# Kernel optimization log

Measured on AMD Instinct MI355X. Metric: run time of the kernel, lower is better.

The kernel has to match this reference:

```python
import jax, jax.numpy as jnp
import numpy as np

BN_EPS = 1e-5

def _bn(x, g, b, m, v):
    # eval-mode BatchNorm1d over channel dim of [B, C, N]
    scale = g / jnp.sqrt(v + BN_EPS)
    return (x - m[:, None]) * scale[:, None] + b[:, None]

def _conv1(W, x, b=None):
    # 1x1 Conv1d == channel matmul: W [O, C], x [B, C, N] -> [B, O, N]
    y = jnp.einsum('oc,bcn->bon', W, x)
    if b is not None:
        y = y + b[:, None]
    return y

def _sa_layer(x, wqk, wv, bv, wt, bt, g, b, m, v):
    # offset self-attention; q_conv and k_conv share weights
    xk = _conv1(wqk, x)                          # [B, D, N]
    xq = jnp.swapaxes(xk, 1, 2)                  # [B, N, D]
    xv = _conv1(wv, x, bv)                       # [B, D, N]
    energy = jnp.einsum('bnd,bdm->bnm', xq, xk)  # [B, N, N]
    attn = jax.nn.softmax(energy, axis=-1)
    attn = attn / (1e-9 + attn.sum(axis=1, keepdims=True))  # L1 renorm over dim=1
    x_r = jnp.einsum('bdn,bnm->bdm', xv, attn)   # [B, D, N]
    x_r = jax.nn.relu(_bn(_conv1(wt, x - x_r, bt), g, b, m, v))
    return x + x_r

def setup_inputs() -> dict:
    key = jax.random.key(0)
    ks = iter(jax.random.split(key, 64))
    B, Cin, N = 16, 3, 2048
    D, F, H1, OUT = 128, 1024, 512, 50
    def rn(shape, s=0.05):
        return jax.random.normal(next(ks), shape, dtype=jnp.float32) * s
    def var(shape):
        return jax.random.uniform(next(ks), shape, dtype=jnp.float32) * 0.5 + 0.5
    inp = {
        'x': jax.random.normal(next(ks), (B, Cin, N), dtype=jnp.float32),
        'w1': rn((D, Cin)), 'w2': rn((D, D)),
        'bn1_g': jnp.ones((D,)), 'bn1_b': jnp.zeros((D,)), 'bn1_m': rn((D,)), 'bn1_v': var((D,)),
        'bn2_g': jnp.ones((D,)), 'bn2_b': jnp.zeros((D,)), 'bn2_m': rn((D,)), 'bn2_v': var((D,)),
        'sa_wqk': rn((4, D, D)), 'sa_wv': rn((4, D, D)), 'sa_bv': rn((4, D)),
        'sa_wt': rn((4, D, D)), 'sa_bt': rn((4, D)),
        'sa_g': jnp.ones((4, D)), 'sa_b': jnp.zeros((4, D)), 'sa_m': rn((4, D)), 'sa_v': var((4, D)),
        'wf': rn((F, 4 * D)),
        'bnf_g': jnp.ones((F,)), 'bnf_b': jnp.zeros((F,)), 'bnf_m': rn((F,)), 'bnf_v': var((F,)),
        'ws1': rn((H1, 3 * F)), 'bs1': rn((H1,)),
        'bns1_g': jnp.ones((H1,)), 'bns1_b': jnp.zeros((H1,)), 'bns1_m': rn((H1,)), 'bns1_v': var((H1,)),
        'ws2': rn((OUT, H1)), 'bs2': rn((OUT,)),
        'bns2_g': jnp.ones((OUT,)), 'bns2_b': jnp.zeros((OUT,)), 'bns2_m': rn((OUT,)), 'bns2_v': var((OUT,)),
    }
    return inp

def reference(x, w1, w2, bn1_g, bn1_b, bn1_m, bn1_v, bn2_g, bn2_b, bn2_m, bn2_v,
              sa_wqk, sa_wv, sa_bv, sa_wt, sa_bt, sa_g, sa_b, sa_m, sa_v,
              wf, bnf_g, bnf_b, bnf_m, bnf_v,
              ws1, bs1, bns1_g, bns1_b, bns1_m, bns1_v,
              ws2, bs2, bns2_g, bns2_b, bns2_m, bns2_v):
    B, _, N = x.shape
    h = jax.nn.relu(_bn(_conv1(w1, x), bn1_g, bn1_b, bn1_m, bn1_v))
    h = jax.nn.relu(_bn(_conv1(w2, h), bn2_g, bn2_b, bn2_m, bn2_v))
    feats = []
    for i in range(4):
        h = _sa_layer(h, sa_wqk[i], sa_wv[i], sa_bv[i], sa_wt[i], sa_bt[i],
                      sa_g[i], sa_b[i], sa_m[i], sa_v[i])
        feats.append(h)
    cat = jnp.concatenate(feats, axis=1)                 # [B, 512, N]
    fused = _bn(_conv1(wf, cat), bnf_g, bnf_b, bnf_m, bnf_v)
    fused = jnp.where(fused >= 0, fused, 0.2 * fused)    # LeakyReLU(0.2)
    x_max = fused.max(axis=2)                            # [B, 1024]
    x_avg = fused.mean(axis=2)                           # [B, 1024]
    gmax = jnp.broadcast_to(x_max[:, :, None], (B, x_max.shape[1], N))
    gavg = jnp.broadcast_to(x_avg[:, :, None], (B, x_avg.shape[1], N))
    h = jnp.concatenate([fused, gmax, gavg], axis=1)     # [B, 3072, N]
    h = jax.nn.relu(_bn(_conv1(ws1, h, bs1), bns1_g, bns1_b, bns1_m, bns1_v))
    # dropout is identity in eval mode
    h = jax.nn.relu(_bn(_conv1(ws2, h, bs2), bns2_g, bns2_b, bns2_m, bns2_v))
    return h  # [B, out_channel, N]
```

## Files before the change

### kernel.cpp

```cpp
#include <hip/hip_runtime.h>
#include <cstdint>
#include <cstddef>

#define B_   16
#define N_   2048
#define D_   128
#define F_   1024
#define H1_  512
#define OUT_ 50

static constexpr float BN_EPS = 1e-5f;

typedef __attribute__((ext_vector_type(8))) short short8;
typedef __attribute__((ext_vector_type(4))) float f32x4;

__device__ inline unsigned short f2bf(float f) {
  union { float f; unsigned u; } v; v.f = f;
  unsigned r = v.u + 0x7fff + ((v.u >> 16) & 1);
  return (unsigned short)(r >> 16);
}

__device__ inline void dma16(const unsigned short* g, unsigned short* l) {
  __builtin_amdgcn_global_load_lds(
      (const __attribute__((address_space(1))) unsigned int*)g,
      (__attribute__((address_space(3))) unsigned int*)l, 16, 0, 0);
}

__global__ void foldw_k(const float* __restrict__ W, int ldW,
                        const float* __restrict__ bias,
                        const float* __restrict__ g, const float* __restrict__ bb,
                        const float* __restrict__ m, const float* __restrict__ v,
                        unsigned short* __restrict__ Wb, float* __restrict__ biasF,
                        int O, int Opad, int K) {
  long i = (long)blockIdx.x * 256 + threadIdx.x;
  if (i >= (long)Opad * K) return;
  int o = (int)(i / K), k = (int)(i % K);
  float sc = 1.f, sh = 0.f;
  if (o < O && g) { sc = g[o] * rsqrtf(v[o] + BN_EPS); sh = bb[o] - m[o] * sc; }
  float w = (o < O) ? W[(long)o * ldW + k] * sc : 0.f;
  Wb[i] = f2bf(w);
  if (k == 0 && biasF) {
    float bf = 0.f;
    if (o < O) bf = (bias ? bias[o] : 0.f) * sc + sh;
    biasF[o] = bf;
  }
}

__global__ void conv1_k(const float* __restrict__ x, const float* __restrict__ w1,
                        const float* __restrict__ g, const float* __restrict__ bb,
                        const float* __restrict__ m, const float* __restrict__ v,
                        unsigned short* __restrict__ h0b) {
  int o = threadIdx.x, n = blockIdx.x, b = blockIdx.y;
  const float* xb = x + (long)b * 3 * N_;
  float val = w1[o * 3 + 0] * xb[n] + w1[o * 3 + 1] * xb[N_ + n] + w1[o * 3 + 2] * xb[2 * N_ + n];
  float sc = g[o] * rsqrtf(v[o] + BN_EPS);
  val = val * sc + (bb[o] - m[o] * sc);
  h0b[((long)b * N_ + n) * D_ + o] = f2bf(fmaxf(val, 0.f));
}

template <int TM>
__global__ __launch_bounds__(256, 4)
void gemm_tok(const unsigned short* __restrict__ Wb, int ldW,
              const unsigned short* __restrict__ A, long sA, int ldA,
              const float* __restrict__ biasF,
              const float* __restrict__ perBO, int ldPBO,
              const float* __restrict__ res, long sRes, int ldRes,
              float* __restrict__ outF, long sOutF, int ldOutF,
              unsigned short* __restrict__ outH, long sOutH, int ldOutH,
              float* __restrict__ pmax, float* __restrict__ psum,
              int K, int act, int flags) {
  constexpr int MT = TM / 32;
  __shared__ unsigned short lA[TM * 64];
  __shared__ unsigned short lB[128 * 64];
  __shared__ float lpm[4][64], lps[4][64];
  int tid = threadIdx.x;
  int n0 = blockIdx.x * TM, o0 = blockIdx.y * 128, b = blockIdx.z;
  int wave = tid >> 6, lane = tid & 63;
  int wr = wave >> 1, wc = wave & 1;
  int quad = lane >> 4, l15 = lane & 15;
  int rowL = lane >> 3;
  int kseg = (lane & 7) ^ rowL;
  const unsigned short* Ab = A + (long)b * sA + (long)n0 * ldA;
  const unsigned short* Wp = Wb + (long)o0 * ldW;

  f32x4 acc[MT][4];
  #pragma unroll
  for (int i = 0; i < MT; ++i)
    #pragma unroll
    for (int j = 0; j < 4; ++j) acc[i][j] = (f32x4){0.f, 0.f, 0.f, 0.f};

  for (int kc = 0; kc < K; kc += 64) {
    #pragma unroll
    for (int t = 0; t < 4; ++t) {
      int chunk = t * 4 + wave;
      dma16(Wp + (long)(chunk * 8 + rowL) * ldW + kc + kseg * 8, &lB[chunk * 512]);
      if (chunk < TM / 8)
        dma16(Ab + (long)(chunk * 8 + rowL) * ldA + kc + kseg * 8, &lA[chunk * 512]);
    }
    __syncthreads();
    #pragma unroll
    for (int kk = 0; kk < 2; ++kk) {
      short8 af[MT], bf[4];
      #pragma unroll
      for (int mt = 0; mt < MT; ++mt) {
        int r = wr * (TM / 2) + mt * 16 + l15;
        af[mt] = *(const short8*)&lA[r * 64 + (((kk * 4 + quad) ^ (l15 & 7)) * 8)];
      }
      #pragma unroll
      for (int ot = 0; ot < 4; ++ot) {
        int r = wc * 64 + ot * 16 + l15;
        bf[ot] = *(const short8*)&lB[r * 64 + (((kk * 4 + quad) ^ (l15 & 7)) * 8)];
      }
      #pragma unroll
      for (int mt = 0; mt < MT; ++mt)
        #pragma unroll
        for (int ot = 0; ot < 4; ++ot)
          acc[mt][ot] = __builtin_amdgcn_mfma_f32_16x16x32_bf16(bf[ot], af[mt], acc[mt][ot], 0, 0, 0);
    }
    __syncthreads();
  }

  bool doPool = (flags & 32) != 0;
  #pragma unroll
  for (int ot = 0; ot < 4; ++ot) {
    int ob = o0 + wc * 64 + ot * 16 + quad * 4;
    float bi[4] = {0.f, 0.f, 0.f, 0.f};
    if (biasF) { float4 t = *(const float4*)&biasF[ob]; bi[0] = t.x; bi[1] = t.y; bi[2] = t.z; bi[3] = t.w; }
    if (perBO) {
      float4 t = *(const float4*)&perBO[(long)b * ldPBO + ob];
      bi[0] += t.x; bi[1] += t.y; bi[2] += t.z; bi[3] += t.w;
    }
    float pm4[4], ps4[4];
    #pragma unroll
    for (int r = 0; r < 4; ++r) { pm4[r] = -1e30f; ps4[r] = 0.f; }
    #pragma unroll
    for (int mt = 0; mt < MT; ++mt) {
      int n = n0 + wr * (TM / 2) + mt * 16 + l15;
      float vals[4];
      #pragma unroll
      for (int r = 0; r < 4; ++r) {
        float val = acc[mt][ot][r] + bi[r];
        if (act == 1)      val = fmaxf(val, 0.f);
        else if (act == 2) val = (val >= 0.f) ? val : 0.2f * val;
        vals[r] = val;
      }
      if (flags & 16) {
        float4 t = *(const float4*)&res[(long)b * sRes + (long)n * ldRes + ob];
        vals[0] += t.x; vals[1] += t.y; vals[2] += t.z; vals[3] += t.w;
      }
      if (flags & 1)
        *(float4*)&outF[(long)b * sOutF + (long)n * ldOutF + ob] = *(float4*)vals;
      {
        unsigned short t[4];
        #pragma unroll
        for (int r = 0; r < 4; ++r) t[r] = f2bf(vals[r]);
        *(uint2*)&outH[(long)b * sOutH + (long)n * ldOutH + ob] = *(uint2*)&t[0];
      }
      if (doPool) {
        #pragma unroll
        for (int r = 0; r < 4; ++r) { pm4[r] = fmaxf(pm4[r], vals[r]); ps4[r] += vals[r]; }
      }
    }
    if (doPool) {
      #pragma unroll
      for (int r = 0; r < 4; ++r) {
        float m = pm4[r], s = ps4[r];
        m = fmaxf(m, __shfl_xor(m, 1)); s += __shfl_xor(s, 1);
        m = fmaxf(m, __shfl_xor(m, 2)); s += __shfl_xor(s, 2);
        m = fmaxf(m, __shfl_xor(m, 4)); s += __shfl_xor(s, 4);
        m = fmaxf(m, __shfl_xor(m, 8)); s += __shfl_xor(s, 8);
        if (l15 == 0) { lpm[wave][ot * 16 + quad * 4 + r] = m; lps[wave][ot * 16 + quad * 4 + r] = s; }
      }
    }
  }
  if (doPool) {
    __syncthreads();
    if (tid < 128) {
      int wcx = tid >> 6, ol = tid & 63;
      float m = fmaxf(lpm[wcx][ol], lpm[wcx + 2][ol]);
      float s = lps[wcx][ol] + lps[wcx + 2][ol];
      int o = o0 + wcx * 64 + ol;
      pmax[((long)b * 16 + blockIdx.x) * 1024 + o] = m;
      psum[((long)b * 16 + blockIdx.x) * 1024 + o] = s;
    }
  }
}

template <int TM>
__global__ __launch_bounds__(256, 4)
void gemm_chan(const unsigned short* __restrict__ Wb, int ldW,
               const unsigned short* __restrict__ A, long sA, int ldA,
               const float* __restrict__ biasF,
               float* __restrict__ outF, long sOutF, int ldOutF,
               unsigned short* __restrict__ outH, long sOutH, int ldOutH,
               int K, int O, int act) {
  constexpr int MT = TM / 32;
  __shared__ unsigned short lA[TM * 64];
  __shared__ unsigned short lB[128 * 64];
  int tid = threadIdx.x;
  int n0 = blockIdx.x * TM, o0 = blockIdx.y * 128, b = blockIdx.z;
  int wave = tid >> 6, lane = tid & 63;
  int wr = wave >> 1, wc = wave & 1;
  int quad = lane >> 4, l15 = lane & 15;
  int rowL = lane >> 3;
  int kseg = (lane & 7) ^ rowL;
  const unsigned short* Ab = A + (long)b * sA + (long)n0 * ldA;
  const unsigned short* Wp = Wb + (long)o0 * ldW;

  f32x4 acc[MT][4];
  #pragma unroll
  for (int i = 0; i < MT; ++i)
    #pragma unroll
    for (int j = 0; j < 4; ++j) acc[i][j] = (f32x4){0.f, 0.f, 0.f, 0.f};

  for (int kc = 0; kc < K; kc += 64) {
    #pragma unroll
    for (int t = 0; t < 4; ++t) {
      int chunk = t * 4 + wave;
      dma16(Wp + (long)(chunk * 8 + rowL) * ldW + kc + kseg * 8, &lB[chunk * 512]);
      if (chunk < TM / 8)
        dma16(Ab + (long)(chunk * 8 + rowL) * ldA + kc + kseg * 8, &lA[chunk * 512]);
    }
    __syncthreads();
    #pragma unroll
    for (int kk = 0; kk < 2; ++kk) {
      short8 af[MT], bf[4];
      #pragma unroll
      for (int mt = 0; mt < MT; ++mt) {
        int r = wr * (TM / 2) + mt * 16 + l15;
        af[mt] = *(const short8*)&lA[r * 64 + (((kk * 4 + quad) ^ (l15 & 7)) * 8)];
      }
      #pragma unroll
      for (int ot = 0; ot < 4; ++ot) {
        int r = wc * 64 + ot * 16 + l15;
        bf[ot] = *(const short8*)&lB[r * 64 + (((kk * 4 + quad) ^ (l15 & 7)) * 8)];
      }
      #pragma unroll
      for (int mt = 0; mt < MT; ++mt)
        #pragma unroll
        for (int ot = 0; ot < 4; ++ot)
          acc[mt][ot] = __builtin_amdgcn_mfma_f32_16x16x32_bf16(af[mt], bf[ot], acc[mt][ot], 0, 0, 0);
    }
    __syncthreads();
  }

  #pragma unroll
  for (int ot = 0; ot < 4; ++ot) {
    int o = o0 + wc * 64 + ot * 16 + l15;
    if (o >= O) continue;
    float bi = biasF ? biasF[o] : 0.f;
    #pragma unroll
    for (int mt = 0; mt < MT; ++mt) {
      int nb = n0 + wr * (TM / 2) + mt * 16 + quad * 4;
      float vals[4];
      #pragma unroll
      for (int r = 0; r < 4; ++r) {
        float val = acc[mt][ot][r] + bi;
        if (act == 1)      val = fmaxf(val, 0.f);
        else if (act == 2) val = (val >= 0.f) ? val : 0.2f * val;
        vals[r] = val;
      }
      if (outF)
        *(float4*)&outF[(long)b * sOutF + (long)o * ldOutF + nb] = *(float4*)vals;
      if (outH) {
        unsigned short t[4];
        #pragma unroll
        for (int r = 0; r < 4; ++r) t[r] = f2bf(vals[r]);
        *(uint2*)&outH[(long)b * sOutH + (long)o * ldOutH + nb] = *(uint2*)&t[0];
      }
    }
  }
}

__global__ __launch_bounds__(256)
void gram_lw(const unsigned short* __restrict__ xk, long sXk,
             float* __restrict__ lw) {
  __shared__ unsigned short lK[64 * 128];
  int tid = threadIdx.x, wave = tid >> 6, lane = tid & 63;
  int quad = lane >> 4, l15 = lane & 15;
  int rowL4 = lane >> 4, s16 = lane & 15;
  int n0 = blockIdx.x * 64, b = blockIdx.y;
  const unsigned short* Kp = xk + (long)b * sXk;
  short8 afr[4];
  {
    const unsigned short* arow = Kp + (long)(n0 + wave * 16 + l15) * 128;
    #pragma unroll
    for (int kf = 0; kf < 4; ++kf) afr[kf] = *(const short8*)(arow + kf * 32 + quad * 8);
  }
  float runm[4], runs[4];
  #pragma unroll
  for (int r = 0; r < 4; ++r) { runm[r] = -1e30f; runs[r] = 0.f; }

  for (int m0 = 0; m0 < 2048; m0 += 64) {
    __syncthreads();
    #pragma unroll
    for (int t = 0; t < 4; ++t) {
      int c = t * 4 + wave;
      int row = c * 4 + rowL4;
      int gseg = (s16 & 8) | ((s16 ^ (row & 7)) & 7);
      dma16(Kp + (long)(m0 + row) * 128 + gseg * 8, &lK[c * 512]);
    }
    __syncthreads();
    #pragma unroll
    for (int mf = 0; mf < 4; ++mf) {
      f32x4 s = (f32x4){0.f, 0.f, 0.f, 0.f};
      #pragma unroll
      for (int kf = 0; kf < 4; ++kf) {
        int r = mf * 16 + l15, q = kf * 4 + quad;
        int sp = (q & 8) | ((q ^ (r & 7)) & 7);
        short8 bfr = *(const short8*)&lK[r * 128 + sp * 8];
        s = __builtin_amdgcn_mfma_f32_16x16x32_bf16(afr[kf], bfr, s, 0, 0, 0);
      }
      #pragma unroll
      for (int r = 0; r < 4; ++r) {
        float e = s[r];
        float mn = fmaxf(runm[r], e);
        runs[r] = runs[r] * __expf(runm[r] - mn) + __expf(e - mn);
        runm[r] = mn;
      }
    }
  }
  #pragma unroll
  for (int r = 0; r < 4; ++r) {
    float m = runm[r], s = runs[r];
    #pragma unroll
    for (int off = 1; off < 16; off <<= 1) {
      float mo = __shfl_xor(m, off), so = __shfl_xor(s, off);
      float mn = fmaxf(m, mo);
      s = s * __expf(m - mn) + so * __expf(mo - mn);
      m = mn;
    }
    if (l15 == 0) {
      int n = n0 + wave * 16 + quad * 4 + r;
      lw[(long)b * 2048 + n] = m + __logf(s);
    }
  }
}

__global__ __launch_bounds__(256)
void pv_k(const unsigned short* __restrict__ xk, long sXk,
          const unsigned short* __restrict__ xv, long sXv,
          const float* __restrict__ lw,
          const float* __restrict__ li, long sLi, int ldLi,
          unsigned short* __restrict__ xrb, long sXr) {
  __shared__ unsigned short lK[64 * 128];
  __shared__ unsigned short lV[128 * 64];
  __shared__ unsigned short lP[4][16 * 72];
  __shared__ float lwt[64];
  int tid = threadIdx.x, wave = tid >> 6, lane = tid & 63;
  int quad = lane >> 4, l15 = lane & 15;
  int rowL4 = lane >> 4, s16 = lane & 15;
  int rowL8 = lane >> 3, s8 = lane & 7;
  int m0 = blockIdx.x * 64, b = blockIdx.y;
  const unsigned short* Kp = xk + (long)b * sXk;
  const unsigned short* Vp = xv + (long)b * sXv;
  short8 akr[4];
  {
    const unsigned short* arow = Kp + (long)(m0 + wave * 16 + l15) * 128;
    #pragma unroll
    for (int kf = 0; kf < 4; ++kf) akr[kf] = *(const short8*)(arow + kf * 32 + quad * 8);
  }
  f32x4 acc[8];
  #pragma unroll
  for (int dt = 0; dt < 8; ++dt) acc[dt] = (f32x4){0.f, 0.f, 0.f, 0.f};
  float runc[4] = {0.f, 0.f, 0.f, 0.f};

  for (int n0c = 0; n0c < 2048; n0c += 64) {
    __syncthreads();
    #pragma unroll
    for (int t = 0; t < 4; ++t) {
      int cK = t * 4 + wave;
      int rowK = cK * 4 + rowL4;
      int gsegK = (s16 & 8) | ((s16 ^ (rowK & 7)) & 7);
      dma16(Kp + (long)(n0c + rowK) * 128 + gsegK * 8, &lK[cK * 512]);
      int cV = t * 4 + wave;
      int rowV = cV * 8 + rowL8;
      int gsegV = s8 ^ (rowV & 7);
      dma16(Vp + (long)rowV * 2048 + n0c + gsegV * 8, &lV[cV * 512]);
    }
    if (tid < 64) lwt[tid] = lw[(long)b * 2048 + n0c + tid];
    __syncthreads();
    #pragma unroll
    for (int nf = 0; nf < 4; ++nf) {
      f32x4 s = (f32x4){0.f, 0.f, 0.f, 0.f};
      #pragma unroll
      for (int kf = 0; kf < 4; ++kf) {
        int r = nf * 16 + l15, q = kf * 4 + quad;
        int sp = (q & 8) | ((q ^ (r & 7)) & 7);
        short8 bfr = *(const short8*)&lK[r * 128 + sp * 8];
        s = __builtin_amdgcn_mfma_f32_16x16x32_bf16(akr[kf], bfr, s, 0, 0, 0);
      }
      float lwc = lwt[nf * 16 + l15];
      #pragma unroll
      for (int r = 0; r < 4; ++r) {
        float p = __expf(s[r] - lwc);
        runc[r] += p;
        lP[wave][(quad * 4 + r) * 72 + nf * 16 + l15] = f2bf(p);
      }
    }
    __syncthreads();
    #pragma unroll
    for (int kc = 0; kc < 2; ++kc) {
      short8 pa = *(const short8*)&lP[wave][l15 * 72 + kc * 32 + quad * 8];
      #pragma unroll
      for (int dt = 0; dt < 8; ++dt) {
        int r = dt * 16 + l15, q = kc * 4 + quad;
        int sp = q ^ (r & 7);
        short8 vb = *(const short8*)&lV[r * 64 + sp * 8];
        acc[dt] = __builtin_amdgcn_mfma_f32_16x16x32_bf16(pa, vb, acc[dt], 0, 0, 0);
      }
    }
  }
  float inv[4];
  #pragma unroll
  for (int r = 0; r < 4; ++r) {
    float s = runc[r];
    #pragma unroll
    for (int off = 1; off < 16; off <<= 1) s += __shfl_xor(s, off);
    inv[r] = 1.f / (1e-9f + s);
  }
  #pragma unroll
  for (int dt = 0; dt < 8; ++dt) {
    int d = dt * 16 + l15;
    #pragma unroll
    for (int r = 0; r < 4; ++r) {
      int m = m0 + wave * 16 + quad * 4 + r;
      float lv = li[(long)b * sLi + (long)m * ldLi + d];
      xrb[(long)b * sXr + (long)m * 128 + d] = f2bf(lv - acc[dt][r] * inv[r]);
    }
  }
}

__global__ void poolred_k(const float* __restrict__ pmax, const float* __restrict__ psum,
                          float* __restrict__ xmax, float* __restrict__ xavg) {
  int f = blockIdx.x * 256 + threadIdx.x, b = blockIdx.y;
  float mx = -1e30f, s = 0.f;
  #pragma unroll
  for (int t = 0; t < 16; ++t) {
    mx = fmaxf(mx, pmax[((long)b * 16 + t) * 1024 + f]);
    s += psum[((long)b * 16 + t) * 1024 + f];
  }
  xmax[(long)b * 1024 + f] = mx;
  xavg[(long)b * 1024 + f] = s * (1.f / 2048.f);
}

__global__ __launch_bounds__(256)
void poolterm_k(const float* __restrict__ ws1, const float* __restrict__ xmax,
                const float* __restrict__ xavg,
                const float* __restrict__ bg, const float* __restrict__ bv,
                float* __restrict__ pt) {
  int o = blockIdx.x, b = blockIdx.y, tid = threadIdx.x;
  const float* w = ws1 + (long)o * 3072;
  float s = 0.f;
  #pragma unroll
  for (int it = 0; it < 4; ++it) {
    int c = tid + it * 256;
    s += w[1024 + c] * xmax[(long)b * 1024 + c] + w[2048 + c] * xavg[(long)b * 1024 + c];
  }
  #pragma unroll
  for (int off = 32; off; off >>= 1) s += __shfl_xor(s, off);
  __shared__ float rsm[4];
  if ((tid & 63) == 0) rsm[tid >> 6] = s;
  __syncthreads();
  if (tid == 0) {
    float sc = bg[o] * rsqrtf(bv[o] + BN_EPS);
    pt[(long)b * H1_ + o] = sc * (rsm[0] + rsm[1] + rsm[2] + rsm[3]);
  }
}

extern "C" void kernel_launch(void* const* d_in, const int* in_sizes, int n_in,
                              void* d_out, int out_size, void* d_ws, size_t ws_size,
                              hipStream_t stream) {
  const float* x      = (const float*)d_in[0];
  const float* w1     = (const float*)d_in[1];
  const float* w2     = (const float*)d_in[2];
  const float* bn1_g  = (const float*)d_in[3];
  const float* bn1_b  = (const float*)d_in[4];
  const float* bn1_m  = (const float*)d_in[5];
  const float* bn1_v  = (const float*)d_in[6];
  const float* bn2_g  = (const float*)d_in[7];
  const float* bn2_b  = (const float*)d_in[8];
  const float* bn2_m  = (const float*)d_in[9];
  const float* bn2_v  = (const float*)d_in[10];
  const float* sa_wqk = (const float*)d_in[11];
  const float* sa_wv  = (const float*)d_in[12];
  const float* sa_bv  = (const float*)d_in[13];
  const float* sa_wt  = (const float*)d_in[14];
  const float* sa_bt  = (const float*)d_in[15];
  const float* sa_g   = (const float*)d_in[16];
  const float* sa_b   = (const float*)d_in[17];
  const float* sa_m   = (const float*)d_in[18];
  const float* sa_v   = (const float*)d_in[19];
  const float* wf     = (const float*)d_in[20];
  const float* bnf_g  = (const float*)d_in[21];
  const float* bnf_b  = (const float*)d_in[22];
  const float* bnf_m  = (const float*)d_in[23];
  const float* bnf_v  = (const float*)d_in[24];
  const float* ws1    = (const float*)d_in[25];
  const float* bs1    = (const float*)d_in[26];
  const float* bns1_g = (const float*)d_in[27];
  const float* bns1_b = (const float*)d_in[28];
  const float* bns1_m = (const float*)d_in[29];
  const float* bns1_v = (const float*)d_in[30];
  const float* ws2    = (const float*)d_in[31];
  const float* bs2    = (const float*)d_in[32];
  const float* bns2_g = (const float*)d_in[33];
  const float* bns2_b = (const float*)d_in[34];
  const float* bns2_m = (const float*)d_in[35];
  const float* bns2_v = (const float*)d_in[36];
  float* out = (float*)d_out;

  float* ws = (float*)d_ws;
  size_t off = 0;
  auto alloc  = [&](size_t n) { float* p = ws + off; off += (n + 63) & ~(size_t)63; return p; };
  auto allocH = [&](size_t n) { return (unsigned short*)alloc((n + 1) / 2); };

  unsigned short* w2b  = allocH(128 * 128);
  unsigned short* wqkb = allocH(4 * 128 * 128);
  unsigned short* wvb  = allocH(4 * 128 * 128);
  unsigned short* wtb  = allocH(4 * 128 * 128);
  unsigned short* wfb  = allocH((size_t)F_ * 512);
  unsigned short* ws1b = allocH((size_t)H1_ * 1024);
  unsigned short* ws2b = allocH((size_t)128 * 512);
  float* bias_w2 = alloc(128);
  float* bias_v  = alloc(512);
  float* bias_t  = alloc(512);
  float* bias_f  = alloc(1024);
  float* bias_s1 = alloc(512);
  float* bias_s2 = alloc(128);
  float* lwB  = alloc((size_t)16 * 2048);
  float* pmax = alloc((size_t)16 * 16 * 1024);
  float* psum = alloc((size_t)16 * 16 * 1024);
  float* xmaxB = alloc((size_t)16 * 1024);
  float* xavgB = alloc((size_t)16 * 1024);
  float* ptB   = alloc((size_t)16 * 512);
  size_t fixedOff = off;

  const size_t perB = 262144  + 1048576  +
                      131072  + 524288  + 1048576  +
                      131072  + 131072  + 131072 ;
  size_t wsFloats = ws_size / 4;
  int Gb = 1;
  for (int c : {16, 8, 4, 2, 1}) {
    if (fixedOff + (size_t)c * perB + 4096 <= wsFloats) { Gb = c; break; }
  }

  float* h1    = alloc((size_t)Gb * 262144);
  float* feats = alloc((size_t)Gb * 1048576);
  unsigned short* h1b    = allocH((size_t)Gb * 262144);
  unsigned short* featsb = allocH((size_t)Gb * 1048576);
  unsigned short* fusedb = allocH((size_t)Gb * 2097152);
  unsigned short* xkb    = allocH((size_t)Gb * 262144);
  unsigned short* xvb    = allocH((size_t)Gb * 262144);
  unsigned short* xrb    = allocH((size_t)Gb * 262144);
  unsigned short* h0b  = xrb;
  unsigned short* hs1b = featsb;

  foldw_k<<<64, 256, 0, stream>>>(w2, 128, nullptr, bn2_g, bn2_b, bn2_m, bn2_v,
                                  w2b, bias_w2, 128, 128, 128);
  for (int i = 0; i < 4; ++i) {
    foldw_k<<<64, 256, 0, stream>>>(sa_wqk + (size_t)i * 16384, 128, nullptr,
                                    nullptr, nullptr, nullptr, nullptr,
                                    wqkb + (size_t)i * 16384, nullptr, 128, 128, 128);
    foldw_k<<<64, 256, 0, stream>>>(sa_wv + (size_t)i * 16384, 128, sa_bv + i * 128,
                                    nullptr, nullptr, nullptr, nullptr,
                                    wvb + (size_t)i * 16384, bias_v + i * 128, 128, 128, 128);
    foldw_k<<<64, 256, 0, stream>>>(sa_wt + (size_t)i * 16384, 128, sa_bt + i * 128,
                                    sa_g + i * 128, sa_b + i * 128, sa_m + i * 128, sa_v + i * 128,
                                    wtb + (size_t)i * 16384, bias_t + i * 128, 128, 128, 128);
  }
  foldw_k<<<2048, 256, 0, stream>>>(wf, 512, nullptr, bnf_g, bnf_b, bnf_m, bnf_v,
                                    wfb, bias_f, 1024, 1024, 512);
  foldw_k<<<2048, 256, 0, stream>>>(ws1, 3072, bs1, bns1_g, bns1_b, bns1_m, bns1_v,
                                    ws1b, bias_s1, 512, 512, 1024);
  foldw_k<<<256, 256, 0, stream>>>(ws2, 512, bs2, bns2_g, bns2_b, bns2_m, bns2_v,
                                   ws2b, bias_s2, 50, 128, 512);

  const long sAct = 262144, sFeat = 1048576, sFus = 2097152;
  for (int b0 = 0; b0 < B_; b0 += Gb) {
    int g = Gb;
    conv1_k<<<dim3(N_, g), 128, 0, stream>>>(x + (long)b0 * 3 * N_, w1,
                                             bn1_g, bn1_b, bn1_m, bn1_v, h0b);
    gemm_tok<64><<<dim3(32, 1, g), 256, 0, stream>>>(
        w2b, 128, h0b, sAct, 128, bias_w2, nullptr, 0, nullptr, 0, 0,
        h1, sAct, 128, h1b, sAct, 128, nullptr, nullptr, 128, 1, 1);

    for (int i = 0; i < 4; ++i) {
      const unsigned short* lib = (i == 0) ? h1b : featsb + (size_t)(i - 1) * 128;
      const float* liF = (i == 0) ? h1 : feats + (size_t)(i - 1) * 128;
      int ldLi = (i == 0) ? 128 : 512;
      long sLi = (i == 0) ? sAct : sFeat;
      gemm_tok<64><<<dim3(32, 1, g), 256, 0, stream>>>(
          wqkb + (size_t)i * 16384, 128, lib, sLi, ldLi, nullptr, nullptr, 0,
          nullptr, 0, 0, nullptr, 0, 0, xkb, sAct, 128, nullptr, nullptr, 128, 0, 0);
      gemm_chan<64><<<dim3(32, 1, g), 256, 0, stream>>>(
          wvb + (size_t)i * 16384, 128, lib, sLi, ldLi, bias_v + i * 128,
          nullptr, 0, 0, xvb, sAct, 2048, 128, 128, 0);
      gram_lw<<<dim3(32, g), 256, 0, stream>>>(xkb, sAct, lwB);
      pv_k<<<dim3(32, g), 256, 0, stream>>>(xkb, sAct, xvb, sAct, lwB,
                                            liF, sLi, ldLi, xrb, sAct);
      gemm_tok<64><<<dim3(32, 1, g), 256, 0, stream>>>(
          wtb + (size_t)i * 16384, 128, xrb, sAct, 128, bias_t + i * 128, nullptr, 0,
          liF, sLi, ldLi,
          feats + (size_t)i * 128, sFeat, 512,
          featsb + (size_t)i * 128, sFeat, 512, nullptr, nullptr, 128, 1, 1 | 16);
    }

    gemm_tok<128><<<dim3(16, 8, g), 256, 0, stream>>>(
        wfb, 512, featsb, sFeat, 512, bias_f, nullptr, 0, nullptr, 0, 0,
        nullptr, 0, 0, fusedb, sFus, 1024, pmax, psum, 512, 2, 32);
    poolred_k<<<dim3(4, g), 256, 0, stream>>>(pmax, psum, xmaxB, xavgB);
    poolterm_k<<<dim3(512, g), 256, 0, stream>>>(ws1, xmaxB, xavgB, bns1_g, bns1_v, ptB);
    gemm_tok<128><<<dim3(16, 4, g), 256, 0, stream>>>(
        ws1b, 1024, fusedb, sFus, 1024, bias_s1, ptB, 512, nullptr, 0, 0,
        nullptr, 0, 0, hs1b, sFeat, 512, nullptr, nullptr, 1024, 1, 0);
    gemm_chan<64><<<dim3(32, 1, g), 256, 0, stream>>>(
        ws2b, 512, hs1b, sFeat, 512, bias_s2,
        out + (long)b0 * OUT_ * N_, (long)OUT_ * N_, 2048, nullptr, 0, 0,
        512, 50, 1);
  }
}
```

Before: 849.0 us.

## Stage bf16 GEMM epilogue through LDS, swap attention grid order, repad lP

When no fp32 output is requested, gemm_tok now writes its bf16 results into a swizzled LDS tile that reuses the A/B staging buffer, then stores full 16-byte rows to global memory instead of scattered 8-byte stores. Pooling partials are computed in that path as well. The gram and PV kernels swap grid dimensions so batch varies fastest, which changes the block scheduling order. The per-wave P buffer padding drops from 72 to 68. The staging adds a barrier and LDS traffic, and the fp32 path now always writes outF, relying on the flags & 1 callers.

```diff
diff --git a/kernel.cpp b/kernel.cpp
--- a/kernel.cpp
+++ b/kernel.cpp
@@ -70,9 +70,11 @@
               float* __restrict__ pmax, float* __restrict__ psum,
               int K, int act, int flags) {
   constexpr int MT = TM / 32;
-  __shared__ unsigned short lA[TM * 64];
-  __shared__ unsigned short lB[128 * 64];
+  __shared__ unsigned short lAB[TM * 64 + 128 * 64];
   __shared__ float lpm[4][64], lps[4][64];
+  unsigned short* lA = lAB;
+  unsigned short* lB = lAB + TM * 64;
+  unsigned short* lS = lAB;
   int tid = threadIdx.x;
   int n0 = blockIdx.x * TM, o0 = blockIdx.y * 128, b = blockIdx.z;
   int wave = tid >> 6, lane = tid & 63;
@@ -121,6 +123,71 @@
   }
 
   bool doPool = (flags & 32) != 0;
+
+  if (!outF) {
+    #pragma unroll
+    for (int ot = 0; ot < 4; ++ot) {
+      int obL = wc * 64 + ot * 16 + quad * 4;
+      int ob = o0 + obL;
+      float bi[4] = {0.f, 0.f, 0.f, 0.f};
+      if (biasF) { float4 t = *(const float4*)&biasF[ob]; bi[0] = t.x; bi[1] = t.y; bi[2] = t.z; bi[3] = t.w; }
+      if (perBO) {
+        float4 t = *(const float4*)&perBO[(long)b * ldPBO + ob];
+        bi[0] += t.x; bi[1] += t.y; bi[2] += t.z; bi[3] += t.w;
+      }
+      float pm4[4], ps4[4];
+      #pragma unroll
+      for (int r = 0; r < 4; ++r) { pm4[r] = -1e30f; ps4[r] = 0.f; }
+      int g = obL >> 3, go = obL & 7;
+      #pragma unroll
+      for (int mt = 0; mt < MT; ++mt) {
+        int nL = wr * (TM / 2) + mt * 16 + l15;
+        unsigned short t4[4];
+        #pragma unroll
+        for (int r = 0; r < 4; ++r) {
+          float val = acc[mt][ot][r] + bi[r];
+          if (act == 1)      val = fmaxf(val, 0.f);
+          else if (act == 2) val = (val >= 0.f) ? val : 0.2f * val;
+          t4[r] = f2bf(val);
+          if (doPool) { pm4[r] = fmaxf(pm4[r], val); ps4[r] += val; }
+        }
+        int gp = (g & 8) | ((g ^ (nL & 7)) & 7);
+        *(uint2*)&lS[nL * 128 + gp * 8 + go] = *(uint2*)&t4[0];
+      }
+      if (doPool) {
+        #pragma unroll
+        for (int r = 0; r < 4; ++r) {
+          float m = pm4[r], s = ps4[r];
+          m = fmaxf(m, __shfl_xor(m, 1)); s += __shfl_xor(s, 1);
+          m = fmaxf(m, __shfl_xor(m, 2)); s += __shfl_xor(s, 2);
+          m = fmaxf(m, __shfl_xor(m, 4)); s += __shfl_xor(s, 4);
+          m = fmaxf(m, __shfl_xor(m, 8)); s += __shfl_xor(s, 8);
+          if (l15 == 0) { lpm[wave][ot * 16 + quad * 4 + r] = m; lps[wave][ot * 16 + quad * 4 + r] = s; }
+        }
+      }
+    }
+    __syncthreads();
+    {
+      int r0 = tid >> 4, s = tid & 15;
+      #pragma unroll
+      for (int it = 0; it < TM / 16; ++it) {
+        int row = it * 16 + r0;
+        int sp = (s & 8) | ((s ^ (row & 7)) & 7);
+        short8 v = *(const short8*)&lS[row * 128 + sp * 8];
+        *(short8*)&outH[(long)b * sOutH + (long)(n0 + row) * ldOutH + o0 + s * 8] = v;
+      }
+    }
+    if (doPool && tid < 128) {
+      int wcx = tid >> 6, ol = tid & 63;
+      float m = fmaxf(lpm[wcx][ol], lpm[wcx + 2][ol]);
+      float s = lps[wcx][ol] + lps[wcx + 2][ol];
+      int o = o0 + wcx * 64 + ol;
+      pmax[((long)b * 16 + blockIdx.x) * 1024 + o] = m;
+      psum[((long)b * 16 + blockIdx.x) * 1024 + o] = s;
+    }
+    return;
+  }
+
   #pragma unroll
   for (int ot = 0; ot < 4; ++ot) {
     int ob = o0 + wc * 64 + ot * 16 + quad * 4;
@@ -130,9 +197,6 @@
       float4 t = *(const float4*)&perBO[(long)b * ldPBO + ob];
       bi[0] += t.x; bi[1] += t.y; bi[2] += t.z; bi[3] += t.w;
     }
-    float pm4[4], ps4[4];
-    #pragma unroll
-    for (int r = 0; r < 4; ++r) { pm4[r] = -1e30f; ps4[r] = 0.f; }
     #pragma unroll
     for (int mt = 0; mt < MT; ++mt) {
       int n = n0 + wr * (TM / 2) + mt * 16 + l15;
@@ -148,40 +212,13 @@
         float4 t = *(const float4*)&res[(long)b * sRes + (long)n * ldRes + ob];
         vals[0] += t.x; vals[1] += t.y; vals[2] += t.z; vals[3] += t.w;
       }
-      if (flags & 1)
-        *(float4*)&outF[(long)b * sOutF + (long)n * ldOutF + ob] = *(float4*)vals;
+      *(float4*)&outF[(long)b * sOutF + (long)n * ldOutF + ob] = *(float4*)vals;
       {
         unsigned short t[4];
         #pragma unroll
         for (int r = 0; r < 4; ++r) t[r] = f2bf(vals[r]);
         *(uint2*)&outH[(long)b * sOutH + (long)n * ldOutH + ob] = *(uint2*)&t[0];
       }
-      if (doPool) {
-        #pragma unroll
-        for (int r = 0; r < 4; ++r) { pm4[r] = fmaxf(pm4[r], vals[r]); ps4[r] += vals[r]; }
-      }
-    }
-    if (doPool) {
-      #pragma unroll
-      for (int r = 0; r < 4; ++r) {
-        float m = pm4[r], s = ps4[r];
-        m = fmaxf(m, __shfl_xor(m, 1)); s += __shfl_xor(s, 1);
-        m = fmaxf(m, __shfl_xor(m, 2)); s += __shfl_xor(s, 2);
-        m = fmaxf(m, __shfl_xor(m, 4)); s += __shfl_xor(s, 4);
-        m = fmaxf(m, __shfl_xor(m, 8)); s += __shfl_xor(s, 8);
-        if (l15 == 0) { lpm[wave][ot * 16 + quad * 4 + r] = m; lps[wave][ot * 16 + quad * 4 + r] = s; }
-      }
-    }
-  }
-  if (doPool) {
-    __syncthreads();
-    if (tid < 128) {
-      int wcx = tid >> 6, ol = tid & 63;
-      float m = fmaxf(lpm[wcx][ol], lpm[wcx + 2][ol]);
-      float s = lps[wcx][ol] + lps[wcx + 2][ol];
-      int o = o0 + wcx * 64 + ol;
-      pmax[((long)b * 16 + blockIdx.x) * 1024 + o] = m;
-      psum[((long)b * 16 + blockIdx.x) * 1024 + o] = s;
     }
   }
 }
@@ -279,7 +316,7 @@
   int tid = threadIdx.x, wave = tid >> 6, lane = tid & 63;
   int quad = lane >> 4, l15 = lane & 15;
   int rowL4 = lane >> 4, s16 = lane & 15;
-  int n0 = blockIdx.x * 64, b = blockIdx.y;
+  int n0 = blockIdx.y * 64, b = blockIdx.x;
   const unsigned short* Kp = xk + (long)b * sXk;
   short8 afr[4];
   {
@@ -345,13 +382,13 @@
           unsigned short* __restrict__ xrb, long sXr) {
   __shared__ unsigned short lK[64 * 128];
   __shared__ unsigned short lV[128 * 64];
-  __shared__ unsigned short lP[4][16 * 72];
+  __shared__ unsigned short lP[4][16 * 68];
   __shared__ float lwt[64];
   int tid = threadIdx.x, wave = tid >> 6, lane = tid & 63;
   int quad = lane >> 4, l15 = lane & 15;
   int rowL4 = lane >> 4, s16 = lane & 15;
   int rowL8 = lane >> 3, s8 = lane & 7;
-  int m0 = blockIdx.x * 64, b = blockIdx.y;
+  int m0 = blockIdx.y * 64, b = blockIdx.x;
   const unsigned short* Kp = xk + (long)b * sXk;
   const unsigned short* Vp = xv + (long)b * sXv;
   short8 akr[4];
@@ -395,13 +432,13 @@
       for (int r = 0; r < 4; ++r) {
         float p = __expf(s[r] - lwc);
         runc[r] += p;
-        lP[wave][(quad * 4 + r) * 72 + nf * 16 + l15] = f2bf(p);
+        lP[wave][(quad * 4 + r) * 68 + nf * 16 + l15] = f2bf(p);
       }
     }
     __syncthreads();
     #pragma unroll
     for (int kc = 0; kc < 2; ++kc) {
-      short8 pa = *(const short8*)&lP[wave][l15 * 72 + kc * 32 + quad * 8];
+      short8 pa = *(const short8*)&lP[wave][l15 * 68 + kc * 32 + quad * 8];
       #pragma unroll
       for (int dt = 0; dt < 8; ++dt) {
         int r = dt * 16 + l15, q = kc * 4 + quad;
@@ -536,9 +573,8 @@
   float* ptB   = alloc((size_t)16 * 512);
   size_t fixedOff = off;
 
-  const size_t perB = 262144  + 1048576  +
-                      131072  + 524288  + 1048576  +
-                      131072  + 131072  + 131072 ;
+  const size_t perB = 262144 + 1048576 + 131072 + 524288 + 1048576 +
+                      131072 + 131072 + 131072;
   size_t wsFloats = ws_size / 4;
   int Gb = 1;
   for (int c : {16, 8, 4, 2, 1}) {
@@ -596,8 +632,8 @@
       gemm_chan<64><<<dim3(32, 1, g), 256, 0, stream>>>(
           wvb + (size_t)i * 16384, 128, lib, sLi, ldLi, bias_v + i * 128,
           nullptr, 0, 0, xvb, sAct, 2048, 128, 128, 0);
-      gram_lw<<<dim3(32, g), 256, 0, stream>>>(xkb, sAct, lwB);
-      pv_k<<<dim3(32, g), 256, 0, stream>>>(xkb, sAct, xvb, sAct, lwB,
+      gram_lw<<<dim3(g, 32), 256, 0, stream>>>(xkb, sAct, lwB);
+      pv_k<<<dim3(g, 32), 256, 0, stream>>>(xkb, sAct, xvb, sAct, lwB,
                                             liF, sLi, ldLi, xrb, sAct);
       gemm_tok<64><<<dim3(32, 1, g), 256, 0, stream>>>(
           wtb + (size_t)i * 16384, 128, xrb, sAct, 128, bias_t + i * 128, nullptr, 0,
```

Result: faster. 827.2 us (-2.6%).
